# Kernel optimization log

Measured on AMD Instinct MI355X. Metric: run time of the kernel, lower is better.

## Reference

```python
import jax, jax.numpy as jnp
import numpy as np

N = 100000   # nodes
E = 5000000  # edges (avg degree 50)
H = 16       # hidden dim


def gcn_conv(x, edge_index, edge_weight, W, b, num_nodes):
    """PyG GCNConv with edge weights: add self-loops (weight 1), symmetric
    normalization deg^-1/2 * w * deg^-1/2, linear transform, scatter-add."""
    row, col = edge_index[0], edge_index[1]  # source j -> target i
    loop = jnp.arange(num_nodes, dtype=edge_index.dtype)
    row = jnp.concatenate([row, loop])
    col = jnp.concatenate([col, loop])
    w = jnp.concatenate([edge_weight, jnp.ones((num_nodes,), edge_weight.dtype)])
    deg = jax.ops.segment_sum(w, col, num_segments=num_nodes)
    dinv = jnp.where(deg > 0, jax.lax.rsqrt(jnp.where(deg > 0, deg, 1.0)), 0.0)
    norm = dinv[row] * w * dinv[col]               # [E+N]
    h = x @ W                                      # [N, out]
    msg = norm[:, None] * h[row]                   # gather + scale
    out = jax.ops.segment_sum(msg, col, num_segments=num_nodes)  # scatter-add
    return out + b


def setup_inputs() -> dict:
    key = jax.random.key(0)
    k = jax.random.split(key, 7)
    x = jax.random.normal(k[0], (N, 1), dtype=jnp.float32)
    edge_index = jax.random.randint(k[1], (2, E), 0, N, dtype=jnp.int32)
    edge_attr = jax.random.uniform(k[2], (E,), dtype=jnp.float32)
    W1 = jax.random.normal(k[3], (1, H), dtype=jnp.float32) * (1.0 / np.sqrt(1.0))
    b1 = jnp.zeros((H,), dtype=jnp.float32)
    W2 = jax.random.normal(k[4], (H, 1), dtype=jnp.float32) * (1.0 / np.sqrt(H))
    b2 = jnp.zeros((1,), dtype=jnp.float32)
    return {"x": x, "edge_index": edge_index, "edge_attr": edge_attr,
            "W1": W1, "b1": b1, "W2": W2, "b2": b2}


def reference(x, edge_index, edge_attr, W1, b1, W2, b2):
    h = gcn_conv(x, edge_index, edge_attr, W1, b1, N)
    h = jax.nn.relu(h)
    out = gcn_conv(h, edge_index, edge_attr, W2, b2, N)
    return out
```

## Files before the change

kernel.cpp:

```cpp
#include <hip/hip_runtime.h>

#define T       256
#define BSHIFT  12
#define BSIZE   4096
#define MAXNB   32
#define M       32
#define EPB     4096
#define EPT     (EPB / T)

__global__ void k_count(const int* __restrict__ col, int* __restrict__ cntT,
                        int E, int nb, int ebp) {
    __shared__ int hist[MAXNB];
    int t = threadIdx.x, g = blockIdx.x;
    if (t < MAXNB) hist[t] = 0;
    __syncthreads();
    int base = g * EPB;
    bool full = (base + EPB <= E);
    if (full) {
#pragma unroll
        for (int k = 0; k < EPT / 4; ++k) {
            int4 c = *(const int4*)(col + base + (t + k * T) * 4);
            atomicAdd(&hist[c.x >> BSHIFT], 1);
            atomicAdd(&hist[c.y >> BSHIFT], 1);
            atomicAdd(&hist[c.z >> BSHIFT], 1);
            atomicAdd(&hist[c.w >> BSHIFT], 1);
        }
    } else {
        for (int k = 0; k < EPT; ++k) {
            int e = base + t + k * T;
            if (e < E) atomicAdd(&hist[col[e] >> BSHIFT], 1);
        }
    }
    __syncthreads();
    if (t < nb) cntT[t * ebp + g] = hist[t];
}

__global__ void k_scan(const int* __restrict__ cntT, int* __restrict__ ofsT,
                       int* __restrict__ tot, int eb, int ebp) {
    __shared__ int tsum[T];
    __shared__ int carry;
    int b = blockIdx.x, t = threadIdx.x;
    if (t == 0) carry = 0;
    __syncthreads();
    int rounds = (eb + T - 1) / T;
    for (int jr = 0; jr < rounds; ++jr) {
        int idx = jr * T + t;
        int v = (idx < eb) ? cntT[b * ebp + idx] : 0;
        tsum[t] = v;
        __syncthreads();
        for (int d = 1; d < T; d <<= 1) {
            int o = (t >= d) ? tsum[t - d] : 0;
            __syncthreads();
            tsum[t] += o;
            __syncthreads();
        }
        int excl = tsum[t] - v + carry;
        if (idx < eb) ofsT[b * ebp + idx] = excl;
        __syncthreads();
        if (t == 0) carry += tsum[T - 1];
        __syncthreads();
    }
    if (t == 0) tot[b] = carry;
}

__global__ void k_scatter(const int* __restrict__ row, const int* __restrict__ col,
                          const float* __restrict__ w,
                          const int* __restrict__ cntT, const int* __restrict__ ofsT,
                          const int* __restrict__ tot,
                          int2* __restrict__ rec, int E, int nb, int ebp) {
    __shared__ int  lofs[MAXNB + 1];
    __shared__ int  rnk[MAXNB];
    __shared__ int  rbase[MAXNB];
    __shared__ int2 buf[EPB];
    __shared__ unsigned char bkt[EPB];
    int t = threadIdx.x, g = blockIdx.x;
    if (t < MAXNB) rnk[t] = 0;
    if (t < 64) {
        int tv = (t < nb) ? ((tot[t] + 3) & ~3) : 0;
        int incA = tv;
#pragma unroll
        for (int d = 1; d < 32; d <<= 1) {
            int o = __shfl_up(incA, d, 64);
            if (t >= d) incA += o;
        }
        int h = (t < nb) ? cntT[t * ebp + g] : 0;
        int incB = h;
#pragma unroll
        for (int d = 1; d < 32; d <<= 1) {
            int o = __shfl_up(incB, d, 64);
            if (t >= d) incB += o;
        }
        if (t == 0) lofs[0] = 0;
        if (t < nb) {
            lofs[t + 1] = incB;
            rbase[t] = (incA - tv) + ofsT[t * ebp + g];
        }
    }
    __syncthreads();

    int base = g * EPB;
    bool full = (base + EPB <= E);
    if (full) {
#pragma unroll
        for (int k = 0; k < EPT / 4; ++k) {
            int idx = base + (t + k * T) * 4;
            int4   c  = *(const int4*)(col + idx);
            int4   r  = *(const int4*)(row + idx);
            float4 wv = *(const float4*)(w + idx);
            int b, rk, pos;
            b = c.x >> BSHIFT; rk = atomicAdd(&rnk[b], 1); pos = lofs[b] + rk;
            buf[pos] = make_int2(((c.x & (BSIZE-1)) << 17) | r.x, __float_as_int(wv.x));
            bkt[pos] = (unsigned char)b;
            b = c.y >> BSHIFT; rk = atomicAdd(&rnk[b], 1); pos = lofs[b] + rk;
            buf[pos] = make_int2(((c.y & (BSIZE-1)) << 17) | r.y, __float_as_int(wv.y));
            bkt[pos] = (unsigned char)b;
            b = c.z >> BSHIFT; rk = atomicAdd(&rnk[b], 1); pos = lofs[b] + rk;
            buf[pos] = make_int2(((c.z & (BSIZE-1)) << 17) | r.z, __float_as_int(wv.z));
            bkt[pos] = (unsigned char)b;
            b = c.w >> BSHIFT; rk = atomicAdd(&rnk[b], 1); pos = lofs[b] + rk;
            buf[pos] = make_int2(((c.w & (BSIZE-1)) << 17) | r.w, __float_as_int(wv.w));
            bkt[pos] = (unsigned char)b;
        }
    } else {
        for (int k = 0; k < EPT; ++k) {
            int e = base + t + k * T;
            if (e < E) {
                int c = col[e];
                int b = c >> BSHIFT;
                int rk = atomicAdd(&rnk[b], 1);
                int pos = lofs[b] + rk;
                buf[pos] = make_int2(((c & (BSIZE-1)) << 17) | row[e], __float_as_int(w[e]));
                bkt[pos] = (unsigned char)b;
            }
        }
    }
    __syncthreads();
    int total = lofs[nb];
    for (int j = t; j < total; j += T) {
        int b = bkt[j];
        rec[rbase[b] + (j - lofs[b])] = buf[j];
    }
}

template <bool HAS_SRC>
__global__ void k_acc(const int2* __restrict__ rec, const int* __restrict__ tot,
                      const float* __restrict__ src, float* __restrict__ part, int nb) {
    __shared__ float acc[BSIZE];
    __shared__ int   bst[MAXNB];
    int t = threadIdx.x, g = blockIdx.x;
    int b = g / M, m = g % M;
    if (t < 64) {
        int tv = (t < nb) ? ((tot[t] + 3) & ~3) : 0;
        int inc = tv;
#pragma unroll
        for (int d = 1; d < 32; d <<= 1) {
            int o = __shfl_up(inc, d, 64);
            if (t >= d) inc += o;
        }
        if (t < nb) bst[t] = inc - tv;
    }
    for (int j = t; j < BSIZE; j += T) acc[j] = 0.0f;
    __syncthreads();
    int s  = bst[b];
    int tb = tot[b];
    int chunk = ((tb + M - 1) / M + 7) & ~7;
    int lo = s + m * chunk;
    int hi = min(s + tb, lo + chunk);
    const int4* rec4 = (const int4*)rec;
    int i = lo + t * 8;
    for (; i + 7 < hi; i += T * 8) {
        int4 q0 = rec4[(i >> 1) + 0];
        int4 q1 = rec4[(i >> 1) + 1];
        int4 q2 = rec4[(i >> 1) + 2];
        int4 q3 = rec4[(i >> 1) + 3];
        float v0 = __int_as_float(q0.y), v1 = __int_as_float(q0.w);
        float v2 = __int_as_float(q1.y), v3 = __int_as_float(q1.w);
        float v4 = __int_as_float(q2.y), v5 = __int_as_float(q2.w);
        float v6 = __int_as_float(q3.y), v7 = __int_as_float(q3.w);
        if (HAS_SRC) {
            v0 *= src[q0.x & 0x1FFFF]; v1 *= src[q0.z & 0x1FFFF];
            v2 *= src[q1.x & 0x1FFFF]; v3 *= src[q1.z & 0x1FFFF];
            v4 *= src[q2.x & 0x1FFFF]; v5 *= src[q2.z & 0x1FFFF];
            v6 *= src[q3.x & 0x1FFFF]; v7 *= src[q3.z & 0x1FFFF];
        }
        atomicAdd(&acc[((unsigned)q0.x) >> 17], v0);
        atomicAdd(&acc[((unsigned)q0.z) >> 17], v1);
        atomicAdd(&acc[((unsigned)q1.x) >> 17], v2);
        atomicAdd(&acc[((unsigned)q1.z) >> 17], v3);
        atomicAdd(&acc[((unsigned)q2.x) >> 17], v4);
        atomicAdd(&acc[((unsigned)q2.z) >> 17], v5);
        atomicAdd(&acc[((unsigned)q3.x) >> 17], v6);
        atomicAdd(&acc[((unsigned)q3.z) >> 17], v7);
    }
    for (; i < hi; ++i) {
        int2 r = rec[i];
        float v = __int_as_float(r.y);
        if (HAS_SRC) v *= src[r.x & 0x1FFFF];
        atomicAdd(&acc[((unsigned)r.x) >> 17], v);
    }
    __syncthreads();
    float* dst = part + (size_t)g * BSIZE;
    for (int j = t; j < BSIZE; j += T) dst[j] = acc[j];
}

__device__ __forceinline__ float reduceM(const float* __restrict__ part, int n) {
    int b = n >> BSHIFT, o = n & (BSIZE - 1);
    const float* pp = part + (size_t)b * M * BSIZE + o;
    float s = 0.0f;
#pragma unroll
    for (int m = 0; m < M; ++m) s += pp[(size_t)m * BSIZE];
    return s;
}

__global__ void k_red_dinv(const float* __restrict__ part, const float* __restrict__ x,
                           float* __restrict__ dinv, float* __restrict__ p, int N) {
    int i = blockIdx.x * blockDim.x + threadIdx.x;
    if (i < N) {
        float d  = reduceM(part, i) + 1.0f;
        float di = rsqrtf(d);
        dinv[i] = di;
        p[i] = di * x[i];
    }
}

__global__ void k_red_mlp(const float* __restrict__ part, const float* __restrict__ dinv,
                          const float* __restrict__ p,
                          const float* __restrict__ W1, const float* __restrict__ b1,
                          const float* __restrict__ W2,
                          float* __restrict__ q, int N) {
    int i = blockIdx.x * blockDim.x + threadIdx.x;
    if (i < N) {
        float di = dinv[i];
        float s  = di * reduceM(part, i) + di * p[i];
        float acc = 0.0f;
#pragma unroll
        for (int k = 0; k < 16; ++k) {
            float h = fmaxf(s * W1[k] + b1[k], 0.0f);
            acc += h * W2[k];
        }
        q[i] = di * acc;
    }
}

__global__ void k_red_out(const float* __restrict__ part, const float* __restrict__ dinv,
                          const float* __restrict__ q, const float* __restrict__ b2,
                          float* __restrict__ out, int N) {
    int i = blockIdx.x * blockDim.x + threadIdx.x;
    if (i < N) {
        float di = dinv[i];
        out[i] = di * reduceM(part, i) + di * q[i] + b2[0];
    }
}

extern "C" void kernel_launch(void* const* d_in, const int* in_sizes, int n_in,
                              void* d_out, int out_size, void* d_ws, size_t ws_size,
                              hipStream_t stream) {
    const float* x  = (const float*)d_in[0];
    const int*   ei = (const int*)  d_in[1];
    const float* ew = (const float*)d_in[2];
    const float* W1 = (const float*)d_in[3];
    const float* b1 = (const float*)d_in[4];
    const float* W2 = (const float*)d_in[5];
    const float* b2 = (const float*)d_in[6];

    const int N = in_sizes[0];
    const int E = in_sizes[2];
    const int* row = ei;
    const int* col = ei + E;
    const int nb  = (N + BSIZE - 1) >> BSHIFT;
    const int eb  = (E + EPB - 1) / EPB;
    const int ebp = (eb + 63) & ~63;

    char* wsp = (char*)d_ws;
    auto take = [&](size_t bytes) {
        char* r = wsp; wsp += (bytes + 255) & ~(size_t)255; return (void*)r;
    };
    int2*  rec  = (int2*) take((size_t)(E + 4 * MAXNB) * 8);
    float* part = (float*)take((size_t)nb * M * BSIZE * 4);
    float* dinv = (float*)take((size_t)N * 4);
    float* p    = (float*)take((size_t)N * 4);
    float* q    = (float*)take((size_t)N * 4);
    int*   cntT = (int*)  take((size_t)MAXNB * ebp * 4);
    int*   ofsT = (int*)  take((size_t)MAXNB * ebp * 4);
    int*   tot  = (int*)  take(MAXNB * 4);

    float* out = (float*)d_out;

    const int nbk = (N + T - 1) / T;
    const int ab  = nb * M;

    k_count  <<<eb, T, 0, stream>>>(col, cntT, E, nb, ebp);
    k_scan   <<<nb, T, 0, stream>>>(cntT, ofsT, tot, eb, ebp);
    k_scatter<<<eb, T, 0, stream>>>(row, col, ew, cntT, ofsT, tot, rec, E, nb, ebp);

    k_acc<false><<<ab, T, 0, stream>>>(rec, tot, nullptr, part, nb);
    k_red_dinv  <<<nbk, T, 0, stream>>>(part, x, dinv, p, N);

    k_acc<true><<<ab, T, 0, stream>>>(rec, tot, p, part, nb);
    k_red_mlp  <<<nbk, T, 0, stream>>>(part, dinv, p, W1, b1, W2, q, N);

    k_acc<true><<<ab, T, 0, stream>>>(rec, tot, q, part, nb);
    k_red_out  <<<nbk, T, 0, stream>>>(part, dinv, q, b2, out, N);
}
```

Before: 239.1 us.

## Replace shared-memory atomics with per-thread histograms and wave-shuffle scans

The count and scatter kernels now keep a private 16-bit counter per thread per bucket in shared memory, so the LDS atomics on a small contended histogram go away. Per-bucket totals and per-thread offsets come from wave shuffle reductions and scans. The scatter kernel loads col once and derives ranks itself, so it no longer needs the stored bkt array; bucket lookup in the copy-out loop becomes a linear walk over lofs. The block-wide scan in k_scan uses shuffles plus per-wave sums instead of a barrier-heavy Hillis-Steele loop. The cost is more shared memory per block, which may lower occupancy, and a stable per-thread ordering in place of atomic ordering.

```diff
diff --git a/kernel.cpp b/kernel.cpp
--- a/kernel.cpp
+++ b/kernel.cpp
@@ -7,12 +7,13 @@
 #define M       32
 #define EPB     4096
 #define EPT     (EPB / T)
+#define HSTRIDE 260
 
 __global__ void k_count(const int* __restrict__ col, int* __restrict__ cntT,
                         int E, int nb, int ebp) {
-    __shared__ int hist[MAXNB];
-    int t = threadIdx.x, g = blockIdx.x;
-    if (t < MAXNB) hist[t] = 0;
+    __shared__ unsigned short hist[MAXNB][HSTRIDE];
+    int t = threadIdx.x, g = blockIdx.x, lane = t & 63, wid = t >> 6;
+    for (int b = 0; b < nb; ++b) hist[b][t] = 0;
     __syncthreads();
     int base = g * EPB;
     bool full = (base + EPB <= E);
@@ -20,44 +21,51 @@
 #pragma unroll
         for (int k = 0; k < EPT / 4; ++k) {
             int4 c = *(const int4*)(col + base + (t + k * T) * 4);
-            atomicAdd(&hist[c.x >> BSHIFT], 1);
-            atomicAdd(&hist[c.y >> BSHIFT], 1);
-            atomicAdd(&hist[c.z >> BSHIFT], 1);
-            atomicAdd(&hist[c.w >> BSHIFT], 1);
+            ++hist[c.x >> BSHIFT][t];
+            ++hist[c.y >> BSHIFT][t];
+            ++hist[c.z >> BSHIFT][t];
+            ++hist[c.w >> BSHIFT][t];
         }
     } else {
         for (int k = 0; k < EPT; ++k) {
             int e = base + t + k * T;
-            if (e < E) atomicAdd(&hist[col[e] >> BSHIFT], 1);
-        }
-    }
-    __syncthreads();
-    if (t < nb) cntT[t * ebp + g] = hist[t];
+            if (e < E) ++hist[col[e] >> BSHIFT][t];
+        }
+    }
+    __syncthreads();
+    for (int b = wid; b < nb; b += 4) {
+        const unsigned short* hp = &hist[b][lane * 4];
+        int s = (int)hp[0] + hp[1] + hp[2] + hp[3];
+#pragma unroll
+        for (int d = 32; d >= 1; d >>= 1) s += __shfl_xor(s, d, 64);
+        if (lane == 0) cntT[b * ebp + g] = s;
+    }
 }
 
 __global__ void k_scan(const int* __restrict__ cntT, int* __restrict__ ofsT,
                        int* __restrict__ tot, int eb, int ebp) {
-    __shared__ int tsum[T];
+    __shared__ int wsum[4];
     __shared__ int carry;
-    int b = blockIdx.x, t = threadIdx.x;
+    int b = blockIdx.x, t = threadIdx.x, lane = t & 63, wid = t >> 6;
     if (t == 0) carry = 0;
     __syncthreads();
     int rounds = (eb + T - 1) / T;
     for (int jr = 0; jr < rounds; ++jr) {
         int idx = jr * T + t;
         int v = (idx < eb) ? cntT[b * ebp + idx] : 0;
-        tsum[t] = v;
+        int inc = v;
+#pragma unroll
+        for (int d = 1; d < 64; d <<= 1) {
+            int o = __shfl_up(inc, d, 64);
+            if (lane >= d) inc += o;
+        }
+        if (lane == 63) wsum[wid] = inc;
         __syncthreads();
-        for (int d = 1; d < T; d <<= 1) {
-            int o = (t >= d) ? tsum[t - d] : 0;
-            __syncthreads();
-            tsum[t] += o;
-            __syncthreads();
-        }
-        int excl = tsum[t] - v + carry;
-        if (idx < eb) ofsT[b * ebp + idx] = excl;
+        int add = carry;
+        for (int w = 0; w < wid; ++w) add += wsum[w];
+        if (idx < eb) ofsT[b * ebp + idx] = inc - v + add;
         __syncthreads();
-        if (t == 0) carry += tsum[T - 1];
+        if (t == 0) carry += wsum[0] + wsum[1] + wsum[2] + wsum[3];
         __syncthreads();
     }
     if (t == 0) tot[b] = carry;
@@ -68,13 +76,58 @@
                           const int* __restrict__ cntT, const int* __restrict__ ofsT,
                           const int* __restrict__ tot,
                           int2* __restrict__ rec, int E, int nb, int ebp) {
+    __shared__ unsigned short cur[MAXNB][HSTRIDE];
     __shared__ int  lofs[MAXNB + 1];
-    __shared__ int  rnk[MAXNB];
+    __shared__ int  btot[MAXNB];
     __shared__ int  rbase[MAXNB];
     __shared__ int2 buf[EPB];
-    __shared__ unsigned char bkt[EPB];
-    int t = threadIdx.x, g = blockIdx.x;
-    if (t < MAXNB) rnk[t] = 0;
+    int t = threadIdx.x, g = blockIdx.x, lane = t & 63, wid = t >> 6;
+    for (int b = 0; b < nb; ++b) cur[b][t] = 0;
+    __syncthreads();
+
+    int base = g * EPB;
+    bool full = (base + EPB <= E);
+    int4 c0, c1, c2, c3;
+    if (full) {
+        c0 = *(const int4*)(col + base + (t + 0 * T) * 4);
+        c1 = *(const int4*)(col + base + (t + 1 * T) * 4);
+        c2 = *(const int4*)(col + base + (t + 2 * T) * 4);
+        c3 = *(const int4*)(col + base + (t + 3 * T) * 4);
+        ++cur[c0.x >> BSHIFT][t]; ++cur[c0.y >> BSHIFT][t];
+        ++cur[c0.z >> BSHIFT][t]; ++cur[c0.w >> BSHIFT][t];
+        ++cur[c1.x >> BSHIFT][t]; ++cur[c1.y >> BSHIFT][t];
+        ++cur[c1.z >> BSHIFT][t]; ++cur[c1.w >> BSHIFT][t];
+        ++cur[c2.x >> BSHIFT][t]; ++cur[c2.y >> BSHIFT][t];
+        ++cur[c2.z >> BSHIFT][t]; ++cur[c2.w >> BSHIFT][t];
+        ++cur[c3.x >> BSHIFT][t]; ++cur[c3.y >> BSHIFT][t];
+        ++cur[c3.z >> BSHIFT][t]; ++cur[c3.w >> BSHIFT][t];
+    } else {
+        for (int k = 0; k < EPT; ++k) {
+            int e = base + t + k * T;
+            if (e < E) ++cur[col[e] >> BSHIFT][t];
+        }
+    }
+    __syncthreads();
+
+    for (int b = wid; b < nb; b += 4) {
+        unsigned short* hp = &cur[b][lane * 4];
+        int a0 = hp[0], a1 = hp[1], a2 = hp[2], a3 = hp[3];
+        int tsum = a0 + a1 + a2 + a3;
+        int inc = tsum;
+#pragma unroll
+        for (int d = 1; d < 64; d <<= 1) {
+            int o = __shfl_up(inc, d, 64);
+            if (lane >= d) inc += o;
+        }
+        int excl = inc - tsum;
+        hp[0] = (unsigned short)excl;
+        hp[1] = (unsigned short)(excl + a0);
+        hp[2] = (unsigned short)(excl + a0 + a1);
+        hp[3] = (unsigned short)(excl + a0 + a1 + a2);
+        if (lane == 63) btot[b] = inc;
+    }
+    __syncthreads();
+
     if (t < 64) {
         int tv = (t < nb) ? ((tot[t] + 3) & ~3) : 0;
         int incA = tv;
@@ -83,7 +136,7 @@
             int o = __shfl_up(incA, d, 64);
             if (t >= d) incA += o;
         }
-        int h = (t < nb) ? cntT[t * ebp + g] : 0;
+        int h = (t < nb) ? btot[t] : 0;
         int incB = h;
 #pragma unroll
         for (int d = 1; d < 32; d <<= 1) {
@@ -98,46 +151,57 @@
     }
     __syncthreads();
 
-    int base = g * EPB;
-    bool full = (base + EPB <= E);
+    auto place = [&](int c, int r, float wv) {
+        int bb = c >> BSHIFT;
+        int o = cur[bb][t];
+        cur[bb][t] = (unsigned short)(o + 1);
+        int pos = lofs[bb] + o;
+        buf[pos] = make_int2(((c & (BSIZE - 1)) << 17) | r, __float_as_int(wv));
+    };
     if (full) {
-#pragma unroll
-        for (int k = 0; k < EPT / 4; ++k) {
-            int idx = base + (t + k * T) * 4;
-            int4   c  = *(const int4*)(col + idx);
-            int4   r  = *(const int4*)(row + idx);
+        {
+            int idx = base + (t + 0 * T) * 4;
+            int4 r = *(const int4*)(row + idx);
             float4 wv = *(const float4*)(w + idx);
-            int b, rk, pos;
-            b = c.x >> BSHIFT; rk = atomicAdd(&rnk[b], 1); pos = lofs[b] + rk;
-            buf[pos] = make_int2(((c.x & (BSIZE-1)) << 17) | r.x, __float_as_int(wv.x));
-            bkt[pos] = (unsigned char)b;
-            b = c.y >> BSHIFT; rk = atomicAdd(&rnk[b], 1); pos = lofs[b] + rk;
-            buf[pos] = make_int2(((c.y & (BSIZE-1)) << 17) | r.y, __float_as_int(wv.y));
-            bkt[pos] = (unsigned char)b;
-            b = c.z >> BSHIFT; rk = atomicAdd(&rnk[b], 1); pos = lofs[b] + rk;
-            buf[pos] = make_int2(((c.z & (BSIZE-1)) << 17) | r.z, __float_as_int(wv.z));
-            bkt[pos] = (unsigned char)b;
-            b = c.w >> BSHIFT; rk = atomicAdd(&rnk[b], 1); pos = lofs[b] + rk;
-            buf[pos] = make_int2(((c.w & (BSIZE-1)) << 17) | r.w, __float_as_int(wv.w));
-            bkt[pos] = (unsigned char)b;
+            place(c0.x, r.x, wv.x); place(c0.y, r.y, wv.y);
+            place(c0.z, r.z, wv.z); place(c0.w, r.w, wv.w);
+        }
+        {
+            int idx = base + (t + 1 * T) * 4;
+            int4 r = *(const int4*)(row + idx);
+            float4 wv = *(const float4*)(w + idx);
+            place(c1.x, r.x, wv.x); place(c1.y, r.y, wv.y);
+            place(c1.z, r.z, wv.z); place(c1.w, r.w, wv.w);
+        }
+        {
+            int idx = base + (t + 2 * T) * 4;
+            int4 r = *(const int4*)(row + idx);
+            float4 wv = *(const float4*)(w + idx);
+            place(c2.x, r.x, wv.x); place(c2.y, r.y, wv.y);
+            place(c2.z, r.z, wv.z); place(c2.w, r.w, wv.w);
+        }
+        {
+            int idx = base + (t + 3 * T) * 4;
+            int4 r = *(const int4*)(row + idx);
+            float4 wv = *(const float4*)(w + idx);
+            place(c3.x, r.x, wv.x); place(c3.y, r.y, wv.y);
+            place(c3.z, r.z, wv.z); place(c3.w, r.w, wv.w);
         }
     } else {
         for (int k = 0; k < EPT; ++k) {
             int e = base + t + k * T;
             if (e < E) {
                 int c = col[e];
-                int b = c >> BSHIFT;
-                int rk = atomicAdd(&rnk[b], 1);
-                int pos = lofs[b] + rk;
-                buf[pos] = make_int2(((c & (BSIZE-1)) << 17) | row[e], __float_as_int(w[e]));
-                bkt[pos] = (unsigned char)b;
+                place(c, row[e], w[e]);
             }
         }
     }
     __syncthreads();
+
     int total = lofs[nb];
+    int b = 0;
     for (int j = t; j < total; j += T) {
-        int b = bkt[j];
+        while (j >= lofs[b + 1]) ++b;
         rec[rbase[b] + (j - lofs[b])] = buf[j];
     }
 }
```

Result: slower. 251.0 us (+5.0%).
